# Performance work log

Hardware: AMD Instinct MI355X
Metric: run time of the kernel (lower is better)

Reference implementation:

```python
import jax, jax.numpy as jnp
import numpy as np

EOS_IDX = 2
B, S, T = 512, 64, 32
V, E, H, DENC, L = 128, 256, 512, 1024, 2


def setup_inputs() -> dict:
    key = jax.random.key(0)
    ks = jax.random.split(key, 24)
    s = 0.02
    inp = {
        "encoder_out": jax.random.normal(ks[0], (B, S, DENC), jnp.float32),
        "h0": jax.random.normal(ks[1], (L, B, H), jnp.float32),
        "c0": jax.random.normal(ks[2], (L, B, H), jnp.float32),
        "targets": jax.random.randint(ks[3], (B, T), 0, V),
        "mask": jax.random.randint(ks[4], (B, S), 0, 2).astype(jnp.int32),
        # parameters
        "emb": jax.random.normal(ks[5], (V, E), jnp.float32) * s,
        "W_enc": jax.random.normal(ks[6], (H, DENC), jnp.float32) * s,
        "W_dec": jax.random.normal(ks[7], (H, H), jnp.float32) * s,
        "v": jax.random.normal(ks[8], (H,), jnp.float32) * s,
        "W_ih0": jax.random.normal(ks[9], (4 * H, E + DENC), jnp.float32) * s,
        "W_hh0": jax.random.normal(ks[10], (4 * H, H), jnp.float32) * s,
        "b_ih0": jax.random.normal(ks[11], (4 * H,), jnp.float32) * s,
        "b_hh0": jax.random.normal(ks[12], (4 * H,), jnp.float32) * s,
        "W_ih1": jax.random.normal(ks[13], (4 * H, H), jnp.float32) * s,
        "W_hh1": jax.random.normal(ks[14], (4 * H, H), jnp.float32) * s,
        "b_ih1": jax.random.normal(ks[15], (4 * H,), jnp.float32) * s,
        "b_hh1": jax.random.normal(ks[16], (4 * H,), jnp.float32) * s,
        "W_out": jax.random.normal(ks[17], (V, H + DENC + E), jnp.float32) * s,
        "b_out": jax.random.normal(ks[18], (V,), jnp.float32) * s,
    }
    # guarantee at least one valid source position per row
    inp["mask"] = inp["mask"].at[:, 0].set(1)
    return inp


def _lstm_cell(x, h, c, W_ih, W_hh, b_ih, b_hh):
    gates = x @ W_ih.T + b_ih + h @ W_hh.T + b_hh  # (B, 4H)
    i, f, g, o = jnp.split(gates, 4, axis=-1)      # torch gate order i,f,g,o
    c_new = jax.nn.sigmoid(f) * c + jax.nn.sigmoid(i) * jnp.tanh(g)
    h_new = jax.nn.sigmoid(o) * jnp.tanh(c_new)
    return h_new, c_new


def reference(encoder_out, h0, c0, targets, mask,
              emb, W_enc, W_dec, v,
              W_ih0, W_hh0, b_ih0, b_hh0,
              W_ih1, W_hh1, b_ih1, b_hh1,
              W_out, b_out):
    # teacher_forcing_ratio = 1.0: input tokens are [EOS, targets[:, :-1]]
    tokens = jnp.concatenate(
        [jnp.full((targets.shape[0], 1), EOS_IDX, dtype=targets.dtype),
         targets[:, :-1]], axis=1)                       # (B, T)
    embedded = emb[tokens]                               # (B, T, E)
    enc_proj = jnp.einsum('bsd,hd->bsh', encoder_out, W_enc)  # precompute W_enc(encoder_out)
    mask_b = mask > 0                                    # (B, S)

    def step(carry, x_emb):                              # x_emb: (B, E)
        h, c = carry                                     # each (L, B, H)
        h_top = h[-1]                                    # (B, H)
        dec_proj = h_top @ W_dec.T                       # (B, H)
        energy = jnp.tanh(dec_proj[:, None, :] + enc_proj)   # (B, S, H)
        score = jnp.einsum('bsh,h->bs', energy, v)       # (B, S)
        score = jnp.where(mask_b, score, -jnp.inf)
        weights = jax.nn.softmax(score, axis=-1)         # (B, S)
        context = jnp.einsum('bs,bsd->bd', weights, encoder_out)  # (B, DENC)
        x = jnp.concatenate([x_emb, context], axis=-1)   # (B, E+DENC)
        h0n, c0n = _lstm_cell(x, h[0], c[0], W_ih0, W_hh0, b_ih0, b_hh0)
        h1n, c1n = _lstm_cell(h0n, h[1], c[1], W_ih1, W_hh1, b_ih1, b_hh1)
        pred = jnp.concatenate([h1n, context, x_emb], axis=-1) @ W_out.T + b_out  # (B, V)
        return (jnp.stack([h0n, h1n]), jnp.stack([c0n, c1n])), pred

    (_, _), preds = jax.lax.scan(step, (h0, c0), jnp.swapaxes(embedded, 0, 1))
    return jnp.swapaxes(preds, 0, 1)                     # (B, T, V)
```

## Files before the change

### kernel.cpp

```cpp
#include <hip/hip_runtime.h>
#include <math.h>

#define BB 512
#define SS 64
#define TT 32
#define VV 128
#define EE 256
#define HH 512
#define DENC 1024
#define BH (BB*HH)
#define XW0 1792
#define XW1 1024
#define PW  1792
#define G4H 2048

typedef __attribute__((ext_vector_type(8))) short bf16x8;
typedef __attribute__((ext_vector_type(4))) short bf16x4;
typedef __attribute__((ext_vector_type(4))) float f32x4;

__device__ __forceinline__ float sigf(float x){ return 1.f/(1.f+expf(-x)); }
__device__ __forceinline__ float bf2f(short s){
  return __uint_as_float(((unsigned)(unsigned short)s) << 16);
}
__device__ __forceinline__ short f2bf(float f){
  unsigned u = __float_as_uint(f);
  return (short)((u + 0x7FFF + ((u>>16)&1)) >> 16);
}
__device__ __forceinline__ float tanh_fast(float x){
  x = fminf(fmaxf(x, -15.f), 15.f);
  float e = __expf(2.f*x);
  return (e - 1.f) / (e + 1.f);
}

__device__ __forceinline__ void zacc(f32x4 a[2][2]){
  #pragma unroll
  for (int i = 0; i < 2; ++i)
    #pragma unroll
    for (int j = 0; j < 2; ++j) a[i][j] = {0.f,0.f,0.f,0.f};
}

template<int BM, int BN>
struct GemmPipe {
  static constexpr int LA = 72;
  static __device__ __forceinline__ void run(short* Asb, short* Bsb,
      const short* __restrict__ A, const short* __restrict__ Bt,
      int lda, int ldb, int kBase, int nIter,
      int rowBase, int colBase, int tid, f32x4 acc[BM/32][BN/32])
  {
    constexpr int FI = BM/32, FJ = BN/32, ACH = BM/32, BCH = BN/32;
    const int lane = tid & 63, wave = tid >> 6;
    const int ml = lane & 15, kq = lane >> 4;
    const int wm = (wave >> 1)*(BM/2), wn = (wave & 1)*(BN/2);
    const int arow = (tid*ACH) >> 3, acol = ((tid*ACH) & 7)*8;
    const int brow = (tid*BCH) >> 3, bcol = ((tid*BCH) & 7)*8;
    const short* Ap = A + (size_t)(rowBase+arow)*lda + kBase + acol;
    const short* Bp = Bt + (size_t)(colBase+brow)*ldb + kBase + bcol;
    bf16x8 ar[ACH], br[BCH];
    #pragma unroll
    for (int c = 0; c < ACH; ++c) ar[c] = *(const bf16x8*)(Ap + c*8);
    #pragma unroll
    for (int c = 0; c < BCH; ++c) br[c] = *(const bf16x8*)(Bp + c*8);
    for (int i = 0; i < nIter; ++i) {
      short* Ab = Asb + (i&1)*(BM*LA);
      short* Bb = Bsb + (i&1)*(BN*LA);
      #pragma unroll
      for (int c = 0; c < ACH; ++c) *(bf16x8*)&Ab[arow*LA + acol + c*8] = ar[c];
      #pragma unroll
      for (int c = 0; c < BCH; ++c) *(bf16x8*)&Bb[brow*LA + bcol + c*8] = br[c];
      __syncthreads();
      if (i+1 < nIter) {
        const short* An = Ap + (size_t)(i+1)*64;
        const short* Bn = Bp + (size_t)(i+1)*64;
        #pragma unroll
        for (int c = 0; c < ACH; ++c) ar[c] = *(const bf16x8*)(An + c*8);
        #pragma unroll
        for (int c = 0; c < BCH; ++c) br[c] = *(const bf16x8*)(Bn + c*8);
      }
      #pragma unroll
      for (int kh = 0; kh < 2; ++kh) {
        bf16x8 af[FI], bfv[FJ];
        #pragma unroll
        for (int ii = 0; ii < FI; ++ii)
          af[ii] = *(const bf16x8*)&Ab[(wm + ii*16 + ml)*LA + kh*32 + kq*8];
        #pragma unroll
        for (int jj = 0; jj < FJ; ++jj)
          bfv[jj] = *(const bf16x8*)&Bb[(wn + jj*16 + ml)*LA + kh*32 + kq*8];
        #pragma unroll
        for (int ii = 0; ii < FI; ++ii)
          #pragma unroll
          for (int jj = 0; jj < FJ; ++jj)
            acc[ii][jj] = __builtin_amdgcn_mfma_f32_16x16x32_bf16(af[ii], bfv[jj], acc[ii][jj], 0,0,0);
      }
    }
    __syncthreads();
  }
};


__device__ __forceinline__ void attn_role(int aid, int tid, char* smem, int t,
    const short* __restrict__ enc_proj, const short* __restrict__ enc_out,
    const float* __restrict__ vvec, const int* __restrict__ mask,
    const int* __restrict__ targets, const short* __restrict__ embb,
    const short* __restrict__ hb, const short* __restrict__ wdecT,
    short* __restrict__ xcat0, short* __restrict__ predcat)
{
  const int b0 = aid*2;
  float* hbf = (float*)smem;
  float* dps = (float*)(smem + 4096);
  float* vvf = (float*)(smem + 12288);
  float* sc  = (float*)(smem + 14336);
  float* wt  = (float*)(smem + 14848);
  {
    bf16x4 h4 = *(const bf16x4*)&hb[(size_t)b0*HH + tid*4];
    #pragma unroll
    for (int j = 0; j < 4; ++j) hbf[tid*4 + j] = bf2f(h4[j]);
    vvf[tid] = vvec[tid];
    vvf[256 + tid] = vvec[256 + tid];
  }
  __syncthreads();
  {
    int unit = tid & 127, ksel = tid >> 7;
    int bb = unit >> 6, h8 = unit & 63;
    const short* wp = wdecT + (size_t)(ksel*256)*HH + h8*8;
    const float* hrow = hbf + bb*HH + ksel*256;
    float a[8] = {0.f,0.f,0.f,0.f,0.f,0.f,0.f,0.f};
    for (int k = 0; k < 256; ++k) {
      bf16x8 w8 = *(const bf16x8*)(wp + (size_t)k*HH);
      float x = hrow[k];
      #pragma unroll
      for (int j = 0; j < 8; ++j) a[j] += x * bf2f(w8[j]);
    }
    float* d = dps + (ksel*2 + bb)*HH + h8*8;
    #pragma unroll
    for (int j = 0; j < 8; ++j) d[j] = a[j];
  }
  __syncthreads();
  {
    int bb = tid >> 7, h0_ = (tid & 127)*4;
    f32x4 s0 = *(f32x4*)&dps[bb*HH + h0_];
    f32x4 s1 = *(f32x4*)&dps[(2 + bb)*HH + h0_];
    *(f32x4*)&dps[bb*HH + h0_] = s0 + s1;
  }
  __syncthreads();
  {
    int u = tid >> 1, khalf = tid & 1;
    int bb = u >> 6, s = u & 63;
    const short* ep = enc_proj + ((size_t)(b0+bb)*SS + s)*HH + khalf*256;
    const float* dpp = dps + bb*HH + khalf*256;
    const float* vp  = vvf + khalf*256;
    float accv = 0.f;
    for (int hc = 0; hc < 32; ++hc) {
      bf16x8 e8 = *(const bf16x8*)(ep + hc*8);
      f32x4 d0 = *(const f32x4*)(dpp + hc*8);
      f32x4 d1 = *(const f32x4*)(dpp + hc*8 + 4);
      f32x4 v0 = *(const f32x4*)(vp + hc*8);
      f32x4 v1 = *(const f32x4*)(vp + hc*8 + 4);
      #pragma unroll
      for (int j = 0; j < 4; ++j) accv += v0[j]*tanh_fast(d0[j] + bf2f(e8[j]));
      #pragma unroll
      for (int j = 0; j < 4; ++j) accv += v1[j]*tanh_fast(d1[j] + bf2f(e8[4+j]));
    }
    accv += __shfl_xor(accv, 1, 64);
    if (khalf == 0) sc[bb*64 + s] = accv;
  }
  __syncthreads();
  if (tid < 128) {
    int bb = tid >> 6, s = tid & 63;
    int valid = mask[(b0+bb)*SS + s];
    float x = valid ? sc[bb*64 + s] : -INFINITY;
    float mx = x;
    #pragma unroll
    for (int off = 32; off; off >>= 1) mx = fmaxf(mx, __shfl_xor(mx, off, 64));
    float e = valid ? __expf(x - mx) : 0.f;
    float sum = e;
    #pragma unroll
    for (int off = 32; off; off >>= 1) sum += __shfl_xor(sum, off, 64);
    wt[bb*64 + s] = e / sum;
  }
  __syncthreads();
  {
    int bb = tid >> 7, d0 = (tid & 127)*8;
    const short* eob = enc_out + (size_t)(b0+bb)*SS*DENC + d0;
    float ca[8] = {0.f,0.f,0.f,0.f,0.f,0.f,0.f,0.f};
    for (int s = 0; s < SS; ++s) {
      float w = wt[bb*64 + s];
      bf16x8 e8 = *(const bf16x8*)(eob + (size_t)s*DENC);
      #pragma unroll
      for (int j = 0; j < 8; ++j) ca[j] += w * bf2f(e8[j]);
    }
    bf16x8 cb8;
    #pragma unroll
    for (int j = 0; j < 8; ++j) cb8[j] = f2bf(ca[j]);
    int b_ = b0 + bb;
    *(bf16x8*)&xcat0[(size_t)b_*XW0 + EE + d0] = cb8;
    *(bf16x8*)&predcat[(size_t)b_*PW + HH + d0] = cb8;
  }
  #pragma unroll
  for (int bb = 0; bb < 2; ++bb) {
    int b_ = b0 + bb;
    int tok = (t == 0) ? 2 : targets[b_*TT + t - 1];
    predcat[(size_t)b_*PW + HH + DENC + tid] = embb[tok*EE + tid];
  }
}

__device__ __forceinline__ void out_role(int idx, int tid, char* smem,
    const short* __restrict__ predprev, const short* __restrict__ wout,
    const float* __restrict__ b_out, float* __restrict__ out, int t)
{
  short* As = (short*)smem;
  short* Bs = (short*)(smem + 18432);
  const int rowBase = (idx >> 1)*64, colBase = (idx & 1)*64;
  f32x4 acc[2][2];
  zacc(acc);
  GemmPipe<64,64>::run(As, Bs, predprev, wout, PW, PW, 0, PW/64, rowBase, colBase, tid, acc);
  const int lane = tid & 63, wave = tid >> 6, ml = lane & 15, kq = lane >> 4;
  const int wm = (wave >> 1)*32, wn = (wave & 1)*32;
  #pragma unroll
  for (int ii = 0; ii < 2; ++ii)
    #pragma unroll
    for (int jj = 0; jj < 2; ++jj) {
      int n = colBase + wn + jj*16 + ml;
      float bv = b_out[n];
      #pragma unroll
      for (int r2 = 0; r2 < 4; ++r2) {
        int m = rowBase + wm + ii*16 + kq*4 + r2;
        out[(size_t)m*(TT*VV) + (size_t)(t-1)*VV + n] = acc[ii][jj][r2] + bv;
      }
    }
}

__device__ __forceinline__ void pstore(int tid, int rowBase, int colBase,
    float* __restrict__ P, f32x4 acc[2][2])
{
  const int lane = tid & 63, wave = tid >> 6, ml = lane & 15, kq = lane >> 4;
  const int wm = (wave >> 1)*32, wn = (wave & 1)*32;
  #pragma unroll
  for (int ii = 0; ii < 2; ++ii)
    #pragma unroll
    for (int jj = 0; jj < 2; ++jj)
      #pragma unroll
      for (int r2 = 0; r2 < 4; ++r2)
        P[(size_t)(rowBase + wm + ii*16 + kq*4 + r2)*G4H + colBase + wn + jj*16 + ml] = acc[ii][jj][r2];
}

__device__ __forceinline__ void gates_epi(int tid, int rowBase, int colBase,
    char* smem, f32x4 acc[2][2], const float* __restrict__ bias,
    float* __restrict__ cb,
    short* __restrict__ d1, int ld1, short* __restrict__ d2, int ld2,
    short* __restrict__ d3)
{
  const int lane = tid & 63, wave = tid >> 6, ml = lane & 15, kq = lane >> 4;
  const int wm = (wave >> 1)*32, wn = (wave & 1)*32;
  float* Ct = (float*)smem;
  float bj0 = bias[colBase + wn + ml];
  float bj1 = bias[colBase + wn + 16 + ml];
  #pragma unroll
  for (int ii = 0; ii < 2; ++ii)
    #pragma unroll
    for (int jj = 0; jj < 2; ++jj)
      #pragma unroll
      for (int r2 = 0; r2 < 4; ++r2)
        Ct[(wm + ii*16 + kq*4 + r2)*68 + wn + jj*16 + ml] = acc[ii][jj][r2] + (jj ? bj1 : bj0);
  __syncthreads();
  #pragma unroll
  for (int kk = 0; kk < 4; ++kk) {
    int cidx = tid + kk*256;
    int m = cidx >> 4, hl = cidx & 15;
    float4 gv = *(float4*)&Ct[m*68 + hl*4];
    int b_ = rowBase + m, h_ = (colBase >> 2) + hl;
    float cp = cb[b_*HH + h_];
    float cn = sigf(gv.y)*cp + sigf(gv.x)*tanhf(gv.z);
    float hn = sigf(gv.w)*tanhf(cn);
    cb[b_*HH + h_] = cn;
    short hb16 = f2bf(hn);
    d1[(size_t)b_*ld1 + h_] = hb16;
    d2[(size_t)b_*ld2 + h_] = hb16;
    if (d3) d3[(size_t)b_*HH + h_] = hb16;
  }
}

__device__ __forceinline__ void emb_prewrite(int rowBase, int tid,
    short* __restrict__ xc0n, const int* __restrict__ targets,
    const short* __restrict__ embb, int t)
{
  int b_ = rowBase + (tid >> 2);
  int tok = targets[b_*TT + t];
  const short* src = embb + tok*EE + (tid & 3)*64;
  short* dst = xc0n + (size_t)b_*XW0 + (tid & 3)*64;
  #pragma unroll
  for (int j = 0; j < 8; ++j)
    *(bf16x8*)(dst + j*8) = *(const bf16x8*)(src + j*8);
}


__global__ __launch_bounds__(256)
void attn_pg01(const short* __restrict__ enc_proj, const short* __restrict__ enc_out,
               const float* __restrict__ vvec, const int* __restrict__ mask,
               const int* __restrict__ targets, const short* __restrict__ embb,
               const short* __restrict__ hb, const short* __restrict__ wdecT,
               short* __restrict__ xcat0, short* __restrict__ predcat,
               const short* __restrict__ wcat0, float* __restrict__ P0,
               const short* __restrict__ xcat1, const short* __restrict__ wcat1,
               float* __restrict__ P1,
               const short* __restrict__ predprev, const short* __restrict__ wout,
               float* __restrict__ Pout, int t)
{
  __shared__ __align__(16) char smem[36864];
  const int tid = threadIdx.x, bid = blockIdx.x;
  if (bid < 256) {
    attn_role(bid, tid, smem, t, enc_proj, enc_out, vvec, mask, targets,
              embb, hb, wdecT, xcat0, predcat);
  } else if (bid < 512) {
    short* As = (short*)smem;
    short* Bs = (short*)(smem + 18432);
    int idx = bid - 256;
    int rowBase = (idx >> 5)*64, colBase = (idx & 31)*64;
    f32x4 acc[2][2];
    zacc(acc);
    GemmPipe<64,64>::run(As, Bs, xcat0, wcat0, XW0, XW0, 0,    4, rowBase, colBase, tid, acc);
    GemmPipe<64,64>::run(As, Bs, xcat0, wcat0, XW0, XW0, 1280, 8, rowBase, colBase, tid, acc);
    pstore(tid, rowBase, colBase, P0, acc);
  } else if (bid < 768) {
    short* As = (short*)smem;
    short* Bs = (short*)(smem + 18432);
    int idx = bid - 512;
    int rowBase = (idx >> 5)*64, colBase = (idx & 31)*64;
    f32x4 acc[2][2];
    zacc(acc);
    GemmPipe<64,64>::run(As, Bs, xcat1, wcat1, XW1, XW1, 512, 8, rowBase, colBase, tid, acc);
    pstore(tid, rowBase, colBase, P1, acc);
  } else {
    if (t >= 1) {
      short* As = (short*)smem;
      short* Bs = (short*)(smem + 18432);
      int idx = bid - 768;
      int half = idx >> 4, oIdx = idx & 15;
      int rowBase = (oIdx >> 1)*64, colBase = (oIdx & 1)*64;
      f32x4 acc[2][2];
      zacc(acc);
      GemmPipe<64,64>::run(As, Bs, predprev, wout, PW, PW, half*896, 14,
                           rowBase, colBase, tid, acc);
      const int lane = tid & 63, wave = tid >> 6, ml = lane & 15, kq = lane >> 4;
      const int wm = (wave >> 1)*32, wn = (wave & 1)*32;
      float* Pt = Pout + half*65536;
      #pragma unroll
      for (int ii = 0; ii < 2; ++ii)
        #pragma unroll
        for (int jj = 0; jj < 2; ++jj)
          #pragma unroll
          for (int r2 = 0; r2 < 4; ++r2)
            Pt[(rowBase + wm + ii*16 + kq*4 + r2)*VV + colBase + wn + jj*16 + ml] = acc[ii][jj][r2];
    }
  }
}

__global__ __launch_bounds__(256)
void gates0_fin(const short* __restrict__ A, const short* __restrict__ W,
                const float* __restrict__ bias, const float* __restrict__ P0,
                float* __restrict__ cb,
                short* __restrict__ d1, short* __restrict__ d2,
                short* __restrict__ xc0n, const int* __restrict__ targets,
                const short* __restrict__ embb,
                const float* __restrict__ Pout, const float* __restrict__ b_out,
                float* __restrict__ out, int t)
{
  __shared__ __align__(16) char smem[36864];
  const int tid = threadIdx.x, bid = blockIdx.x;
  if (bid >= 264) {
    if (t >= 1) {
      int base = (bid - 264)*8192 + tid*32;
      #pragma unroll
      for (int j = 0; j < 8; ++j) {
        int i = base + j*4;
        f32x4 a = *(const f32x4*)&Pout[i];
        f32x4 b = *(const f32x4*)&Pout[65536 + i];
        int m = i >> 7, n = i & 127;
        f32x4 bo = *(const f32x4*)&b_out[n];
        f32x4 r = a + b + bo;
        *(f32x4*)&out[(size_t)m*(TT*VV) + (size_t)(t-1)*VV + n] = r;
      }
    }
    return;
  }
  if (bid >= 256) {
    if (t + 1 < TT) emb_prewrite((bid - 256)*64, tid, xc0n, targets, embb, t);
    return;
  }
  short* As = (short*)smem;
  short* Bs = (short*)(smem + 18432);
  const int rowBase = (bid >> 5)*64, colBase = (bid & 31)*64;
  const int lane = tid & 63, wave = tid >> 6, ml = lane & 15, kq = lane >> 4;
  const int wm = (wave >> 1)*32, wn = (wave & 1)*32;
  f32x4 acc[2][2];
  const float* Pp = P0 + (size_t)rowBase*G4H + colBase;
  #pragma unroll
  for (int ii = 0; ii < 2; ++ii)
    #pragma unroll
    for (int jj = 0; jj < 2; ++jj)
      #pragma unroll
      for (int r2 = 0; r2 < 4; ++r2)
        acc[ii][jj][r2] = Pp[(wm + ii*16 + kq*4 + r2)*G4H + wn + jj*16 + ml];
  GemmPipe<64,64>::run(As, Bs, A, W, XW0, XW0, 256, 16, rowBase, colBase, tid, acc);
  gates_epi(tid, rowBase, colBase, smem, acc, bias, cb, d1, XW1, d2, XW0, (short*)nullptr);
}

__global__ __launch_bounds__(256)
void gates1_fin(const short* __restrict__ A, const short* __restrict__ W,
                const float* __restrict__ bias, const float* __restrict__ P1,
                float* __restrict__ cb,
                short* __restrict__ d1, short* __restrict__ d2, short* __restrict__ d3)
{
  __shared__ __align__(16) char smem[36864];
  const int tid = threadIdx.x, bid = blockIdx.x;
  short* As = (short*)smem;
  short* Bs = (short*)(smem + 18432);
  const int rowBase = (bid >> 5)*64, colBase = (bid & 31)*64;
  const int lane = tid & 63, wave = tid >> 6, ml = lane & 15, kq = lane >> 4;
  const int wm = (wave >> 1)*32, wn = (wave & 1)*32;
  f32x4 acc[2][2];
  const float* Pp = P1 + (size_t)rowBase*G4H + colBase;
  #pragma unroll
  for (int ii = 0; ii < 2; ++ii)
    #pragma unroll
    for (int jj = 0; jj < 2; ++jj)
      #pragma unroll
      for (int r2 = 0; r2 < 4; ++r2)
        acc[ii][jj][r2] = Pp[(wm + ii*16 + kq*4 + r2)*G4H + wn + jj*16 + ml];
  GemmPipe<64,64>::run(As, Bs, A, W, XW1, XW1, 0, 8, rowBase, colBase, tid, acc);
  gates_epi(tid, rowBase, colBase, smem, acc, bias, cb, d1, XW1, d2, PW, d3);
}

__global__ __launch_bounds__(256)
void out_fin(const short* __restrict__ predprev, const short* __restrict__ wout,
             const float* __restrict__ b_out, float* __restrict__ out)
{
  __shared__ __align__(16) char smem[36864];
  out_role(blockIdx.x, threadIdx.x, smem, predprev, wout, b_out, out, TT);
}

__global__ __launch_bounds__(256)
void enc_gemm(short* __restrict__ C, const short* __restrict__ A, const short* __restrict__ Bt,
              int K, int ldc)
{
  __shared__ __align__(16) char smem[55296];
  short* As = (short*)smem;
  short* Bs = (short*)(smem + 18432);
  const int tid = threadIdx.x;
  const int rowBase = blockIdx.y*64, colBase = blockIdx.x*128;
  f32x4 acc[2][4];
  #pragma unroll
  for (int i = 0; i < 2; ++i)
    #pragma unroll
    for (int j = 0; j < 4; ++j) acc[i][j] = {0.f,0.f,0.f,0.f};
  GemmPipe<64,128>::run(As, Bs, A, Bt, K, K, 0, K >> 6, rowBase, colBase, tid, acc);
  const int lane = tid & 63, wave = tid >> 6, ml = lane & 15, kq = lane >> 4;
  const int wm = (wave >> 1)*32, wn = (wave & 1)*64;
  #pragma unroll
  for (int ii = 0; ii < 2; ++ii)
    #pragma unroll
    for (int jj = 0; jj < 4; ++jj) {
      int n = colBase + wn + jj*16 + ml;
      #pragma unroll
      for (int r2 = 0; r2 < 4; ++r2) {
        int m = rowBase + wm + ii*16 + kq*4 + r2;
        C[(size_t)m*ldc + n] = f2bf(acc[ii][jj][r2]);
      }
    }
}

__global__ __launch_bounds__(256)
void build_wcat_bf(short* __restrict__ wcat0, short* __restrict__ wcat1,
                   const float* __restrict__ wih0, const float* __restrict__ whh0,
                   const float* __restrict__ wih1, const float* __restrict__ whh1)
{
  int idx = blockIdx.x*256 + threadIdx.x;
  const int N0 = G4H*XW0;
  if (idx < N0) {
    int n = idx / XW0, k = idx % XW0;
    int row = (n & 3)*HH + (n >> 2);
    float v = (k < EE+DENC) ? wih0[(size_t)row*(EE+DENC) + k] : whh0[(size_t)row*HH + (k - (EE+DENC))];
    wcat0[idx] = f2bf(v);
  } else {
    int j = idx - N0;
    int n = j / XW1, k = j % XW1;
    int row = (n & 3)*HH + (n >> 2);
    float v = (k < HH) ? wih1[(size_t)row*HH + k] : whh1[(size_t)row*HH + (k - HH)];
    wcat1[j] = f2bf(v);
  }
}

__global__ __launch_bounds__(256)
void cvt_encout(short* __restrict__ dst, const float* __restrict__ src)
{
  size_t i8 = ((size_t)blockIdx.x*256 + threadIdx.x)*8;
  float4 a = *(const float4*)&src[i8];
  float4 b = *(const float4*)&src[i8+4];
  bf16x8 o;
  o[0]=f2bf(a.x); o[1]=f2bf(a.y); o[2]=f2bf(a.z); o[3]=f2bf(a.w);
  o[4]=f2bf(b.x); o[5]=f2bf(b.y); o[6]=f2bf(b.z); o[7]=f2bf(b.w);
  *(bf16x8*)&dst[i8] = o;
}

__global__ __launch_bounds__(256)
void prep_misc(float* __restrict__ cbuf, short* __restrict__ xcat0a, short* __restrict__ xcat1a,
               short* __restrict__ hb, short* __restrict__ wdecT, short* __restrict__ wenc,
               short* __restrict__ wout, short* __restrict__ embb,
               float* __restrict__ bias0i, float* __restrict__ bias1i,
               const float* __restrict__ c0, const float* __restrict__ h0,
               const float* __restrict__ W_dec, const float* __restrict__ W_enc,
               const float* __restrict__ W_out, const float* __restrict__ emb,
               const float* __restrict__ b_ih0, const float* __restrict__ b_hh0,
               const float* __restrict__ b_ih1, const float* __restrict__ b_hh1)
{
  int idx = blockIdx.x*256 + threadIdx.x;
  if (idx < 524288) { cbuf[idx] = c0[idx]; return; }
  idx -= 524288;
  if (idx < 262144) {
    int b = idx >> 9, h = idx & 511;
    xcat0a[(size_t)b*XW0 + EE + DENC + h] = f2bf(h0[idx]);
    return;
  }
  idx -= 262144;
  if (idx < 262144) {
    int b = idx >> 9, h = idx & 511;
    short v = f2bf(h0[BH + idx]);
    xcat1a[(size_t)b*XW1 + HH + h] = v;
    hb[idx] = v;
    return;
  }
  idx -= 262144;
  if (idx < 262144) {
    int k = idx >> 9, n = idx & 511;
    wdecT[idx] = f2bf(W_dec[(size_t)n*HH + k]);
    return;
  }
  idx -= 262144;
  if (idx < 524288) { wenc[idx] = f2bf(W_enc[idx]); return; }
  idx -= 524288;
  if (idx < 229376) { wout[idx] = f2bf(W_out[idx]); return; }
  idx -= 229376;
  if (idx < 32768)  { embb[idx] = f2bf(emb[idx]); return; }
  idx -= 32768;
  if (idx < 2048) {
    int row = (idx & 3)*HH + (idx >> 2);
    bias0i[idx] = b_ih0[row] + b_hh0[row];
    return;
  }
  idx -= 2048;
  if (idx < 2048) {
    int row = (idx & 3)*HH + (idx >> 2);
    bias1i[idx] = b_ih1[row] + b_hh1[row];
    return;
  }
  idx -= 2048;
  {
    int b = idx >> 8, e = idx & 255;
    xcat0a[(size_t)b*XW0 + e] = f2bf(emb[2*EE + e]);
  }
}

extern "C" void kernel_launch(void* const* d_in, const int* in_sizes, int n_in,
                              void* d_out, int out_size, void* d_ws, size_t ws_size,
                              hipStream_t stream) {
  const float* enc_out = (const float*)d_in[0];
  const float* h0      = (const float*)d_in[1];
  const float* c0      = (const float*)d_in[2];
  const int*   targets = (const int*)d_in[3];
  const int*   mask    = (const int*)d_in[4];
  const float* emb     = (const float*)d_in[5];
  const float* W_enc   = (const float*)d_in[6];
  const float* W_dec   = (const float*)d_in[7];
  const float* v       = (const float*)d_in[8];
  const float* b_ih0   = (const float*)d_in[11];
  const float* b_hh0   = (const float*)d_in[12];
  const float* b_ih1   = (const float*)d_in[15];
  const float* b_hh1   = (const float*)d_in[16];
  const float* b_out   = (const float*)d_in[18];
  float* out = (float*)d_out;

  char* ws = (char*)d_ws;
  size_t o = 0;
  short* enc_out_bf = (short*)(ws + o); o += (size_t)BB*SS*DENC*2;
  short* enc_proj_bf= (short*)(ws + o); o += (size_t)BB*SS*HH*2;
  short* wcat0i     = (short*)(ws + o); o += (size_t)G4H*XW0*2;
  short* wcat1i     = (short*)(ws + o); o += (size_t)G4H*XW1*2;
  short* wdecT      = (short*)(ws + o); o += (size_t)HH*HH*2;
  short* wenc_bf    = (short*)(ws + o); o += (size_t)HH*DENC*2;
  short* wout_bf    = (short*)(ws + o); o += (size_t)VV*PW*2;
  short* emb_bf     = (short*)(ws + o); o += (size_t)VV*EE*2;
  short* xcat0a     = (short*)(ws + o); o += (size_t)BB*XW0*2;
  short* xcat0b     = (short*)(ws + o); o += (size_t)BB*XW0*2;
  short* xcat1a     = (short*)(ws + o); o += (size_t)BB*XW1*2;
  short* xcat1b     = (short*)(ws + o); o += (size_t)BB*XW1*2;
  short* predcata   = (short*)(ws + o); o += (size_t)BB*PW*2;
  short* predcatb   = (short*)(ws + o); o += (size_t)BB*PW*2;
  short* hb         = (short*)(ws + o); o += (size_t)BH*2;
  float* cbuf       = (float*)(ws + o); o += (size_t)2*BH*4;
  float* bias0i     = (float*)(ws + o); o += (size_t)G4H*4;
  float* bias1i     = (float*)(ws + o); o += (size_t)G4H*4;
  float* P0         = (float*)(ws + o); o += (size_t)BB*G4H*4;
  float* P1         = (float*)(ws + o); o += (size_t)BB*G4H*4;
  float* Pout       = (float*)(ws + o); o += (size_t)2*BB*VV*4;
  (void)ws_size; (void)in_sizes; (void)n_in; (void)out_size;

  cvt_encout<<<16384, 256, 0, stream>>>(enc_out_bf, enc_out);
  build_wcat_bf<<<22528, 256, 0, stream>>>(wcat0i, wcat1i,
      (const float*)d_in[9], (const float*)d_in[10], (const float*)d_in[13], (const float*)d_in[14]);
  prep_misc<<<8720, 256, 0, stream>>>(cbuf, xcat0a, xcat1a, hb, wdecT, wenc_bf, wout_bf, emb_bf,
      bias0i, bias1i, c0, h0, W_dec, W_enc, (const float*)d_in[17], emb,
      b_ih0, b_hh0, b_ih1, b_hh1);
  enc_gemm<<<dim3(HH/128, (BB*SS)/64), 256, 0, stream>>>(
      enc_proj_bf, enc_out_bf, wenc_bf, DENC, HH);

  short* xc0[2] = {xcat0a, xcat0b};
  short* xc1[2] = {xcat1a, xcat1b};
  short* pc[2]  = {predcata, predcatb};
  for (int t = 0; t < TT; ++t) {
    attn_pg01<<<800, 256, 0, stream>>>(enc_proj_bf, enc_out_bf, v, mask, targets, emb_bf,
        hb, wdecT, xc0[t&1], pc[t&1], wcat0i, P0, xc1[t&1], wcat1i, P1,
        pc[(t+1)&1], wout_bf, Pout, t);
    gates0_fin<<<272, 256, 0, stream>>>(
        xc0[t&1], wcat0i, bias0i, P0, cbuf, xc1[t&1], xc0[(t+1)&1] + EE + DENC,
        xc0[(t+1)&1], targets, emb_bf, Pout, b_out, out, t);
    gates1_fin<<<256, 256, 0, stream>>>(
        xc1[t&1], wcat1i, bias1i, P1, cbuf + BH, xc1[(t+1)&1] + HH, pc[t&1], hb);
  }
  out_fin<<<16, 256, 0, stream>>>(pc[1], wout_bf, b_out, out);
}
```

Measured before the change: 2.674 ms.

## Use 128-wide swizzled K tiles in gate GEMMs and split output GEMM 4-way

Adds a GEMM pipeline with a 128-element K step and XOR-swizzled shared memory, used by both gate finalize kernels. This halves loop iterations and barriers and is meant to avoid LDS bank conflicts. The output projection is split into four K partitions instead of two, spreading it over more blocks, with a four-way reduction afterward. Shared memory per block grows to 64KB, which can reduce occupancy, and the partial buffer doubles.

```diff
diff --git a/kernel.cpp b/kernel.cpp
--- a/kernel.cpp
+++ b/kernel.cpp
@@ -85,6 +85,69 @@
         #pragma unroll
         for (int jj = 0; jj < FJ; ++jj)
           bfv[jj] = *(const bf16x8*)&Bb[(wn + jj*16 + ml)*LA + kh*32 + kq*8];
+        #pragma unroll
+        for (int ii = 0; ii < FI; ++ii)
+          #pragma unroll
+          for (int jj = 0; jj < FJ; ++jj)
+            acc[ii][jj] = __builtin_amdgcn_mfma_f32_16x16x32_bf16(af[ii], bfv[jj], acc[ii][jj], 0,0,0);
+      }
+    }
+    __syncthreads();
+  }
+};
+
+template<int BM, int BN>
+struct GemmPipeK {
+  static __device__ __forceinline__ void run(char* Asb, char* Bsb,
+      const short* __restrict__ A, const short* __restrict__ Bt,
+      int lda, int ldb, int kBase, int nIter,
+      int rowBase, int colBase, int tid, f32x4 acc[BM/32][BN/32])
+  {
+    constexpr int FI = BM/32, FJ = BN/32;
+    constexpr int ACH = (BM*128)/(256*8), BCH = (BN*128)/(256*8);
+    const int lane = tid & 63, wave = tid >> 6;
+    const int ml = lane & 15, kq = lane >> 4;
+    const int wm = (wave >> 1)*(BM/2), wn = (wave & 1)*(BN/2);
+    const int arow = (tid*ACH) >> 4, acs = (tid*ACH) & 15;
+    const int brow = (tid*BCH) >> 4, bcs = (tid*BCH) & 15;
+    const short* Ap = A + (size_t)(rowBase+arow)*lda + kBase + acs*8;
+    const short* Bp = Bt + (size_t)(colBase+brow)*ldb + kBase + bcs*8;
+    bf16x8 ar[ACH], br[BCH];
+    #pragma unroll
+    for (int c = 0; c < ACH; ++c) ar[c] = *(const bf16x8*)(Ap + c*8);
+    #pragma unroll
+    for (int c = 0; c < BCH; ++c) br[c] = *(const bf16x8*)(Bp + c*8);
+    for (int i = 0; i < nIter; ++i) {
+      char* Ab = Asb + (i&1)*(BM*256);
+      char* Bb = Bsb + (i&1)*(BN*256);
+      #pragma unroll
+      for (int c = 0; c < ACH; ++c)
+        *(bf16x8*)(Ab + arow*256 + (((acs + c)*16) ^ ((arow & 15) << 4))) = ar[c];
+      #pragma unroll
+      for (int c = 0; c < BCH; ++c)
+        *(bf16x8*)(Bb + brow*256 + (((bcs + c)*16) ^ ((brow & 15) << 4))) = br[c];
+      __syncthreads();
+      if (i+1 < nIter) {
+        const short* An = Ap + (size_t)(i+1)*128;
+        const short* Bn = Bp + (size_t)(i+1)*128;
+        #pragma unroll
+        for (int c = 0; c < ACH; ++c) ar[c] = *(const bf16x8*)(An + c*8);
+        #pragma unroll
+        for (int c = 0; c < BCH; ++c) br[c] = *(const bf16x8*)(Bn + c*8);
+      }
+      #pragma unroll
+      for (int kh = 0; kh < 4; ++kh) {
+        bf16x8 af[FI], bfv[FJ];
+        #pragma unroll
+        for (int ii = 0; ii < FI; ++ii) {
+          int r = wm + ii*16 + ml;
+          af[ii] = *(const bf16x8*)(Ab + r*256 + ((kh*64 + kq*16) ^ ((r & 15) << 4)));
+        }
+        #pragma unroll
+        for (int jj = 0; jj < FJ; ++jj) {
+          int r = wn + jj*16 + ml;
+          bfv[jj] = *(const bf16x8*)(Bb + r*256 + ((kh*64 + kq*16) ^ ((r & 15) << 4)));
+        }
         #pragma unroll
         for (int ii = 0; ii < FI; ++ii)
           #pragma unroll
@@ -334,15 +397,15 @@
       short* As = (short*)smem;
       short* Bs = (short*)(smem + 18432);
       int idx = bid - 768;
-      int half = idx >> 4, oIdx = idx & 15;
+      int q = idx >> 4, oIdx = idx & 15;
       int rowBase = (oIdx >> 1)*64, colBase = (oIdx & 1)*64;
       f32x4 acc[2][2];
       zacc(acc);
-      GemmPipe<64,64>::run(As, Bs, predprev, wout, PW, PW, half*896, 14,
+      GemmPipe<64,64>::run(As, Bs, predprev, wout, PW, PW, q*448, 7,
                            rowBase, colBase, tid, acc);
       const int lane = tid & 63, wave = tid >> 6, ml = lane & 15, kq = lane >> 4;
       const int wm = (wave >> 1)*32, wn = (wave & 1)*32;
-      float* Pt = Pout + half*65536;
+      float* Pt = Pout + q*65536;
       #pragma unroll
       for (int ii = 0; ii < 2; ++ii)
         #pragma unroll
@@ -364,7 +427,7 @@
                 const float* __restrict__ Pout, const float* __restrict__ b_out,
                 float* __restrict__ out, int t)
 {
-  __shared__ __align__(16) char smem[36864];
+  __shared__ __align__(16) char smem[65536];
   const int tid = threadIdx.x, bid = blockIdx.x;
   if (bid >= 264) {
     if (t >= 1) {
@@ -374,9 +437,11 @@
         int i = base + j*4;
         f32x4 a = *(const f32x4*)&Pout[i];
         f32x4 b = *(const f32x4*)&Pout[65536 + i];
+        f32x4 c = *(const f32x4*)&Pout[131072 + i];
+        f32x4 d = *(const f32x4*)&Pout[196608 + i];
         int m = i >> 7, n = i & 127;
         f32x4 bo = *(const f32x4*)&b_out[n];
-        f32x4 r = a + b + bo;
+        f32x4 r = a + b + c + d + bo;
         *(f32x4*)&out[(size_t)m*(TT*VV) + (size_t)(t-1)*VV + n] = r;
       }
     }
@@ -386,8 +451,8 @@
     if (t + 1 < TT) emb_prewrite((bid - 256)*64, tid, xc0n, targets, embb, t);
     return;
   }
-  short* As = (short*)smem;
-  short* Bs = (short*)(smem + 18432);
+  char* As = smem;
+  char* Bs = smem + 32768;
   const int rowBase = (bid >> 5)*64, colBase = (bid & 31)*64;
   const int lane = tid & 63, wave = tid >> 6, ml = lane & 15, kq = lane >> 4;
   const int wm = (wave >> 1)*32, wn = (wave & 1)*32;
@@ -400,7 +465,7 @@
       #pragma unroll
       for (int r2 = 0; r2 < 4; ++r2)
         acc[ii][jj][r2] = Pp[(wm + ii*16 + kq*4 + r2)*G4H + wn + jj*16 + ml];
-  GemmPipe<64,64>::run(As, Bs, A, W, XW0, XW0, 256, 16, rowBase, colBase, tid, acc);
+  GemmPipeK<64,64>::run(As, Bs, A, W, XW0, XW0, 256, 8, rowBase, colBase, tid, acc);
   gates_epi(tid, rowBase, colBase, smem, acc, bias, cb, d1, XW1, d2, XW0, (short*)nullptr);
 }
 
@@ -410,10 +475,10 @@
                 float* __restrict__ cb,
                 short* __restrict__ d1, short* __restrict__ d2, short* __restrict__ d3)
 {
-  __shared__ __align__(16) char smem[36864];
+  __shared__ __align__(16) char smem[65536];
   const int tid = threadIdx.x, bid = blockIdx.x;
-  short* As = (short*)smem;
-  short* Bs = (short*)(smem + 18432);
+  char* As = smem;
+  char* Bs = smem + 32768;
   const int rowBase = (bid >> 5)*64, colBase = (bid & 31)*64;
   const int lane = tid & 63, wave = tid >> 6, ml = lane & 15, kq = lane >> 4;
   const int wm = (wave >> 1)*32, wn = (wave & 1)*32;
@@ -426,7 +491,7 @@
       #pragma unroll
       for (int r2 = 0; r2 < 4; ++r2)
         acc[ii][jj][r2] = Pp[(wm + ii*16 + kq*4 + r2)*G4H + wn + jj*16 + ml];
-  GemmPipe<64,64>::run(As, Bs, A, W, XW1, XW1, 0, 8, rowBase, colBase, tid, acc);
+  GemmPipeK<64,64>::run(As, Bs, A, W, XW1, XW1, 0, 4, rowBase, colBase, tid, acc);
   gates_epi(tid, rowBase, colBase, smem, acc, bias, cb, d1, XW1, d2, PW, d3);
 }
 
@@ -600,7 +665,7 @@
   float* bias1i     = (float*)(ws + o); o += (size_t)G4H*4;
   float* P0         = (float*)(ws + o); o += (size_t)BB*G4H*4;
   float* P1         = (float*)(ws + o); o += (size_t)BB*G4H*4;
-  float* Pout       = (float*)(ws + o); o += (size_t)2*BB*VV*4;
+  float* Pout       = (float*)(ws + o); o += (size_t)4*BB*VV*4;
   (void)ws_size; (void)in_sizes; (void)n_in; (void)out_size;
 
   cvt_encout<<<16384, 256, 0, stream>>>(enc_out_bf, enc_out);
@@ -616,7 +681,7 @@
   short* xc1[2] = {xcat1a, xcat1b};
   short* pc[2]  = {predcata, predcatb};
   for (int t = 0; t < TT; ++t) {
-    attn_pg01<<<800, 256, 0, stream>>>(enc_proj_bf, enc_out_bf, v, mask, targets, emb_bf,
+    attn_pg01<<<832, 256, 0, stream>>>(enc_proj_bf, enc_out_bf, v, mask, targets, emb_bf,
         hb, wdecT, xc0[t&1], pc[t&1], wcat0i, P0, xc1[t&1], wcat1i, P1,
         pc[(t+1)&1], wout_bf, Pout, t);
     gates0_fin<<<272, 256, 0, stream>>>(
```

Result: no change. 2.690 ms (+0.6%).

## Halve gate-finish tile rows and split output projection K four ways

Applied to the files above, without the earlier changes.

The gates0_fin and gates1_fin kernels now use 32x64 tiles instead of 64x64, which doubles their grid to 512 blocks and cuts per-block LDS use. The goal is to fill more compute units on the serial per-timestep critical path. The output-projection partial GEMM is split into four K-slices instead of two, so attn_pg01 launches 32 extra blocks, Pout grows to four partial buffers, and the final sum reads all four. The cost is more partial-sum traffic and smaller tiles with less reuse per block.

```diff
diff --git a/kernel.cpp b/kernel.cpp
--- a/kernel.cpp
+++ b/kernel.cpp
@@ -243,19 +243,20 @@
         P[(size_t)(rowBase + wm + ii*16 + kq*4 + r2)*G4H + colBase + wn + jj*16 + ml] = acc[ii][jj][r2];
 }
 
+template<int BM>
 __device__ __forceinline__ void gates_epi(int tid, int rowBase, int colBase,
-    char* smem, f32x4 acc[2][2], const float* __restrict__ bias,
+    char* smem, f32x4 acc[BM/32][2], const float* __restrict__ bias,
     float* __restrict__ cb,
     short* __restrict__ d1, int ld1, short* __restrict__ d2, int ld2,
     short* __restrict__ d3)
 {
   const int lane = tid & 63, wave = tid >> 6, ml = lane & 15, kq = lane >> 4;
-  const int wm = (wave >> 1)*32, wn = (wave & 1)*32;
+  const int wm = (wave >> 1)*(BM/2), wn = (wave & 1)*32;
   float* Ct = (float*)smem;
   float bj0 = bias[colBase + wn + ml];
   float bj1 = bias[colBase + wn + 16 + ml];
   #pragma unroll
-  for (int ii = 0; ii < 2; ++ii)
+  for (int ii = 0; ii < BM/32; ++ii)
     #pragma unroll
     for (int jj = 0; jj < 2; ++jj)
       #pragma unroll
@@ -263,7 +264,7 @@
         Ct[(wm + ii*16 + kq*4 + r2)*68 + wn + jj*16 + ml] = acc[ii][jj][r2] + (jj ? bj1 : bj0);
   __syncthreads();
   #pragma unroll
-  for (int kk = 0; kk < 4; ++kk) {
+  for (int kk = 0; kk < BM/16; ++kk) {
     int cidx = tid + kk*256;
     int m = cidx >> 4, hl = cidx & 15;
     float4 gv = *(float4*)&Ct[m*68 + hl*4];
@@ -334,15 +335,15 @@
       short* As = (short*)smem;
       short* Bs = (short*)(smem + 18432);
       int idx = bid - 768;
-      int half = idx >> 4, oIdx = idx & 15;
+      int q = idx >> 4, oIdx = idx & 15;
       int rowBase = (oIdx >> 1)*64, colBase = (oIdx & 1)*64;
       f32x4 acc[2][2];
       zacc(acc);
-      GemmPipe<64,64>::run(As, Bs, predprev, wout, PW, PW, half*896, 14,
+      GemmPipe<64,64>::run(As, Bs, predprev, wout, PW, PW, q*448, 7,
                            rowBase, colBase, tid, acc);
       const int lane = tid & 63, wave = tid >> 6, ml = lane & 15, kq = lane >> 4;
       const int wm = (wave >> 1)*32, wn = (wave & 1)*32;
-      float* Pt = Pout + half*65536;
+      float* Pt = Pout + q*65536;
       #pragma unroll
       for (int ii = 0; ii < 2; ++ii)
         #pragma unroll
@@ -364,44 +365,44 @@
                 const float* __restrict__ Pout, const float* __restrict__ b_out,
                 float* __restrict__ out, int t)
 {
-  __shared__ __align__(16) char smem[36864];
+  __shared__ __align__(16) char smem[27648];
   const int tid = threadIdx.x, bid = blockIdx.x;
-  if (bid >= 264) {
+  if (bid >= 520) {
     if (t >= 1) {
-      int base = (bid - 264)*8192 + tid*32;
+      int base = (bid - 520)*8192 + tid*32;
       #pragma unroll
       for (int j = 0; j < 8; ++j) {
         int i = base + j*4;
         f32x4 a = *(const f32x4*)&Pout[i];
         f32x4 b = *(const f32x4*)&Pout[65536 + i];
+        f32x4 c = *(const f32x4*)&Pout[131072 + i];
+        f32x4 d = *(const f32x4*)&Pout[196608 + i];
         int m = i >> 7, n = i & 127;
         f32x4 bo = *(const f32x4*)&b_out[n];
-        f32x4 r = a + b + bo;
+        f32x4 r = a + b + c + d + bo;
         *(f32x4*)&out[(size_t)m*(TT*VV) + (size_t)(t-1)*VV + n] = r;
       }
     }
     return;
   }
-  if (bid >= 256) {
-    if (t + 1 < TT) emb_prewrite((bid - 256)*64, tid, xc0n, targets, embb, t);
+  if (bid >= 512) {
+    if (t + 1 < TT) emb_prewrite((bid - 512)*64, tid, xc0n, targets, embb, t);
     return;
   }
   short* As = (short*)smem;
-  short* Bs = (short*)(smem + 18432);
-  const int rowBase = (bid >> 5)*64, colBase = (bid & 31)*64;
+  short* Bs = (short*)(smem + 9216);
+  const int rowBase = (bid >> 5)*32, colBase = (bid & 31)*64;
   const int lane = tid & 63, wave = tid >> 6, ml = lane & 15, kq = lane >> 4;
-  const int wm = (wave >> 1)*32, wn = (wave & 1)*32;
-  f32x4 acc[2][2];
+  const int wm = (wave >> 1)*16, wn = (wave & 1)*32;
+  f32x4 acc[1][2];
   const float* Pp = P0 + (size_t)rowBase*G4H + colBase;
   #pragma unroll
-  for (int ii = 0; ii < 2; ++ii)
-    #pragma unroll
-    for (int jj = 0; jj < 2; ++jj)
-      #pragma unroll
-      for (int r2 = 0; r2 < 4; ++r2)
-        acc[ii][jj][r2] = Pp[(wm + ii*16 + kq*4 + r2)*G4H + wn + jj*16 + ml];
-  GemmPipe<64,64>::run(As, Bs, A, W, XW0, XW0, 256, 16, rowBase, colBase, tid, acc);
-  gates_epi(tid, rowBase, colBase, smem, acc, bias, cb, d1, XW1, d2, XW0, (short*)nullptr);
+  for (int jj = 0; jj < 2; ++jj)
+    #pragma unroll
+    for (int r2 = 0; r2 < 4; ++r2)
+      acc[0][jj][r2] = Pp[(wm + kq*4 + r2)*G4H + wn + jj*16 + ml];
+  GemmPipe<32,64>::run(As, Bs, A, W, XW0, XW0, 256, 16, rowBase, colBase, tid, acc);
+  gates_epi<32>(tid, rowBase, colBase, smem, acc, bias, cb, d1, XW1, d2, XW0, (short*)nullptr);
 }
 
 __global__ __launch_bounds__(256)
@@ -410,24 +411,22 @@
                 float* __restrict__ cb,
                 short* __restrict__ d1, short* __restrict__ d2, short* __restrict__ d3)
 {
-  __shared__ __align__(16) char smem[36864];
+  __shared__ __align__(16) char smem[27648];
   const int tid = threadIdx.x, bid = blockIdx.x;
   short* As = (short*)smem;
-  short* Bs = (short*)(smem + 18432);
-  const int rowBase = (bid >> 5)*64, colBase = (bid & 31)*64;
+  short* Bs = (short*)(smem + 9216);
+  const int rowBase = (bid >> 5)*32, colBase = (bid & 31)*64;
   const int lane = tid & 63, wave = tid >> 6, ml = lane & 15, kq = lane >> 4;
-  const int wm = (wave >> 1)*32, wn = (wave & 1)*32;
-  f32x4 acc[2][2];
+  const int wm = (wave >> 1)*16, wn = (wave & 1)*32;
+  f32x4 acc[1][2];
   const float* Pp = P1 + (size_t)rowBase*G4H + colBase;
   #pragma unroll
-  for (int ii = 0; ii < 2; ++ii)
-    #pragma unroll
-    for (int jj = 0; jj < 2; ++jj)
-      #pragma unroll
-      for (int r2 = 0; r2 < 4; ++r2)
-        acc[ii][jj][r2] = Pp[(wm + ii*16 + kq*4 + r2)*G4H + wn + jj*16 + ml];
-  GemmPipe<64,64>::run(As, Bs, A, W, XW1, XW1, 0, 8, rowBase, colBase, tid, acc);
-  gates_epi(tid, rowBase, colBase, smem, acc, bias, cb, d1, XW1, d2, PW, d3);
+  for (int jj = 0; jj < 2; ++jj)
+    #pragma unroll
+    for (int r2 = 0; r2 < 4; ++r2)
+      acc[0][jj][r2] = Pp[(wm + kq*4 + r2)*G4H + wn + jj*16 + ml];
+  GemmPipe<32,64>::run(As, Bs, A, W, XW1, XW1, 0, 8, rowBase, colBase, tid, acc);
+  gates_epi<32>(tid, rowBase, colBase, smem, acc, bias, cb, d1, XW1, d2, PW, d3);
 }
 
 __global__ __launch_bounds__(256)
@@ -600,7 +599,7 @@
   float* bias1i     = (float*)(ws + o); o += (size_t)G4H*4;
   float* P0         = (float*)(ws + o); o += (size_t)BB*G4H*4;
   float* P1         = (float*)(ws + o); o += (size_t)BB*G4H*4;
-  float* Pout       = (float*)(ws + o); o += (size_t)2*BB*VV*4;
+  float* Pout       = (float*)(ws + o); o += (size_t)4*BB*VV*4;
   (void)ws_size; (void)in_sizes; (void)n_in; (void)out_size;
 
   cvt_encout<<<16384, 256, 0, stream>>>(enc_out_bf, enc_out);
@@ -616,13 +615,13 @@
   short* xc1[2] = {xcat1a, xcat1b};
   short* pc[2]  = {predcata, predcatb};
   for (int t = 0; t < TT; ++t) {
-    attn_pg01<<<800, 256, 0, stream>>>(enc_proj_bf, enc_out_bf, v, mask, targets, emb_bf,
+    attn_pg01<<<832, 256, 0, stream>>>(enc_proj_bf, enc_out_bf, v, mask, targets, emb_bf,
         hb, wdecT, xc0[t&1], pc[t&1], wcat0i, P0, xc1[t&1], wcat1i, P1,
         pc[(t+1)&1], wout_bf, Pout, t);
-    gates0_fin<<<272, 256, 0, stream>>>(
+    gates0_fin<<<528, 256, 0, stream>>>(
         xc0[t&1], wcat0i, bias0i, P0, cbuf, xc1[t&1], xc0[(t+1)&1] + EE + DENC,
         xc0[(t+1)&1], targets, emb_bf, Pout, b_out, out, t);
-    gates1_fin<<<256, 256, 0, stream>>>(
+    gates1_fin<<<512, 256, 0, stream>>>(
         xc1[t&1], wcat1i, bias1i, P1, cbuf + BH, xc1[(t+1)&1] + HH, pc[t&1], hb);
   }
   out_fin<<<16, 256, 0, stream>>>(pc[1], wout_bf, b_out, out);
```

Result: no change. 2.654 ms (-0.7%).
